# Kernel tuning notes

Measured on AMD Instinct MI355X. Metric: run time of the kernel, lower is better.

The kernel has to match this reference:

```python
import jax, jax.numpy as jnp
import numpy as np

DIM = 256
HEADS = 8
DIM_HEAD = 64
INNER = HEADS * DIM_HEAD  # 512
SCALE = DIM_HEAD ** -0.5


def setup_inputs() -> dict:
    key = jax.random.key(0)
    ks = jax.random.split(key, 6)
    b, n, m = 8, 2048, 16
    x = jax.random.normal(ks[0], (b, n, DIM), dtype=jnp.float32)
    y = jax.random.normal(ks[1], (b, n, m, DIM), dtype=jnp.float32)
    # nn.Linear weights stored as [out, in] in torch; we use [in, out] for x @ W
    W_q = jax.random.normal(ks[2], (DIM, INNER), dtype=jnp.float32) * (DIM ** -0.5)
    W_kv = jax.random.normal(ks[3], (DIM, 2 * INNER), dtype=jnp.float32) * (DIM ** -0.5)
    W_out = jax.random.normal(ks[4], (INNER, DIM), dtype=jnp.float32) * (INNER ** -0.5)
    b_out = jax.random.normal(ks[5], (DIM,), dtype=jnp.float32) * 0.01
    return {"x": x, "y": y, "W_q": W_q, "W_kv": W_kv, "W_out": W_out, "b_out": b_out}


def reference(x, y, W_q, W_kv, W_out, b_out):
    b, n, m, _ = y.shape
    h, d = HEADS, DIM_HEAD
    q = (x @ W_q).reshape(b, n, h, d)                      # [b,n,h,d] (single query per position)
    kv = y @ W_kv                                          # [b,n,m,2*inner]
    k, v = jnp.split(kv, 2, axis=-1)
    k = k.reshape(b, n, m, h, d)
    v = v.reshape(b, n, m, h, d)
    dots = jnp.einsum('bnhd,bnmhd->bnhm', q, k) * SCALE    # scores over m context tokens
    attn = jax.nn.softmax(dots, axis=-1)
    out = jnp.einsum('bnhm,bnmhd->bnhd', attn, v).reshape(b, n, h * d)
    return out @ W_out + b_out                             # [b,n,dim]
```

## Files before the change

kernel.cpp:

```cpp
#include <hip/hip_runtime.h>
#include <cmath>

#define NPOS 16384
#define ATT_SCALE 0.125f

typedef float f4 __attribute__((ext_vector_type(4)));
typedef short short8 __attribute__((ext_vector_type(8)));
typedef unsigned int uint;
typedef unsigned short ushort;

__device__ __forceinline__ ushort f2bf(float f) {
    union { float f; uint u; } v; v.f = f;
    uint r = v.u + 0x7fffu + ((v.u >> 16) & 1u);
    return (ushort)(r >> 16);
}
__device__ __forceinline__ float bfl(uint u) { union { uint u; float f; } v; v.u = u << 16; return v.f; }
__device__ __forceinline__ float bfh(uint u) { union { uint u; float f; } v; v.u = u & 0xffff0000u; return v.f; }

__device__ __forceinline__ void gl_lds16(const ushort* g, ushort* l) {
    __builtin_amdgcn_global_load_lds(
        (const __attribute__((address_space(1))) uint*)g,
        (__attribute__((address_space(3))) uint*)l, 16, 0, 0);
}

template<int BN, bool C_F32, bool BIAS>
__global__ __launch_bounds__(256) void gemm_bt(
    const ushort* __restrict__ A, int lda,
    const ushort* __restrict__ Bt, int ldb,
    void* __restrict__ Cg, int ldc,
    const float* __restrict__ bias, int K)
{
    constexpr int NI = BN / 32;
    __shared__ __align__(16) ushort A_lds[128 * 64];
    __shared__ __align__(16) ushort B_lds[BN * 64];
    const int mt = blockIdx.x, nt = blockIdx.y;
    const int row0 = mt * 128, col0 = nt * BN;
    const int tid = threadIdx.x;
    const int lane = tid & 63, w = tid >> 6;
    const int frow = lane & 15, quad = lane >> 4;
    const int wr = (w >> 1) * 64, wc = (w & 1) * (BN / 2);
    const int srow = lane >> 3;
    const int gch = ((lane & 7) ^ (lane >> 3)) * 8;

    f4 acc[4][NI];
    #pragma unroll
    for (int mi = 0; mi < 4; ++mi)
        #pragma unroll
        for (int ni = 0; ni < NI; ++ni)
            acc[mi][ni] = (f4){0.f, 0.f, 0.f, 0.f};

    for (int k0 = 0; k0 < K; k0 += 64) {
        #pragma unroll
        for (int it = 0; it < 4; ++it) {
            int sr = (it * 4 + w) * 8;
            gl_lds16(A + (size_t)(row0 + sr + srow) * lda + k0 + gch,
                     &A_lds[sr * 64]);
        }
        #pragma unroll
        for (int it = 0; it < BN / 32; ++it) {
            int sr = (it * 4 + w) * 8;
            gl_lds16(Bt + (size_t)(col0 + sr + srow) * ldb + k0 + gch,
                     &B_lds[sr * 64]);
        }
        __syncthreads();

        #pragma unroll
        for (int kk = 0; kk < 2; ++kk) {
            const int ko = (((kk * 4 + quad) ^ (frow & 7)) << 3);
            short8 av[4];
            #pragma unroll
            for (int mi = 0; mi < 4; ++mi)
                av[mi] = *(const short8*)&A_lds[(wr + mi * 16 + frow) * 64 + ko];
            #pragma unroll
            for (int ni = 0; ni < NI; ++ni) {
                short8 bv = *(const short8*)&B_lds[(wc + ni * 16 + frow) * 64 + ko];
                #pragma unroll
                for (int mi = 0; mi < 4; ++mi)
                    acc[mi][ni] = __builtin_amdgcn_mfma_f32_16x16x32_bf16(bv, av[mi], acc[mi][ni], 0, 0, 0);
            }
        }
        __syncthreads();
    }

    #pragma unroll
    for (int mi = 0; mi < 4; ++mi) {
        const int r = row0 + wr + mi * 16 + frow;
        #pragma unroll
        for (int ni = 0; ni < NI; ++ni) {
            const int c = col0 + wc + ni * 16 + quad * 4;
            f4 v = acc[mi][ni];
            if (C_F32) {
                float* C = (float*)Cg;
                if (BIAS) {
                    const float4 bv = *(const float4*)&bias[c];
                    v[0] += bv.x; v[1] += bv.y; v[2] += bv.z; v[3] += bv.w;
                }
                *(float4*)&C[(size_t)r * ldc + c] = make_float4(v[0], v[1], v[2], v[3]);
            } else {
                ushort* C = (ushort*)Cg;
                uint2 pv;
                pv.x = (uint)f2bf(v[0]) | ((uint)f2bf(v[1]) << 16);
                pv.y = (uint)f2bf(v[2]) | ((uint)f2bf(v[3]) << 16);
                *(uint2*)&C[(size_t)r * ldc + c] = pv;
            }
        }
    }
}

__global__ __launch_bounds__(256) void prep_all(
    const float* __restrict__ x, ushort* __restrict__ xb,
    const float* __restrict__ Wq, const float* __restrict__ Wkv,
    const float* __restrict__ Wout,
    ushort* __restrict__ Wf1n, ushort* __restrict__ Wf2t)
{
    __shared__ float As[64][65];
    __shared__ float Bs[64][65];

    if (blockIdx.x >= 256) {
        const int i = ((blockIdx.x - 256) * 256 + threadIdx.x) * 8;
        float4 v0 = *(const float4*)&x[i];
        float4 v1 = *(const float4*)&x[i + 4];
        uint4 p;
        p.x = (uint)f2bf(v0.x) | ((uint)f2bf(v0.y) << 16);
        p.y = (uint)f2bf(v0.z) | ((uint)f2bf(v0.w) << 16);
        p.z = (uint)f2bf(v1.x) | ((uint)f2bf(v1.y) << 16);
        p.w = (uint)f2bf(v1.z) | ((uint)f2bf(v1.w) << 16);
        *(uint4*)&xb[i] = p;
        return;
    }

    const int b = blockIdx.x;
    const bool second = (b >= 128);
    const int bb = second ? b - 128 : b;
    const int h = bb >> 4, ct = (bb >> 2) & 3, et = bb & 3;
    const int t = threadIdx.x;
    const int c0 = ct * 64, e0 = et * 64;
    const int tx = t & 15, ty = t >> 4;

    const float* Ab = Wkv + (second ? 512 : 0) + h * 64;
    #pragma unroll
    for (int it = 0; it < 4; ++it) {
        int idx = t + it * 256;
        int row = idx >> 4, col = (idx & 15) * 4;
        float4 v = *(const float4*)&Ab[(size_t)(c0 + row) * 1024 + col];
        As[row][col] = v.x; As[row][col + 1] = v.y;
        As[row][col + 2] = v.z; As[row][col + 3] = v.w;
    }
    #pragma unroll
    for (int it = 0; it < 4; ++it) {
        int idx = t + it * 256;
        int row = idx >> 4, col = (idx & 15) * 4;
        float4 v;
        if (second)
            v = *(const float4*)&Wout[(size_t)(h * 64 + row) * 256 + e0 + col];
        else
            v = *(const float4*)&Wq[(size_t)(e0 + row) * 512 + h * 64 + col];
        Bs[row][col] = v.x; Bs[row][col + 1] = v.y;
        Bs[row][col + 2] = v.z; Bs[row][col + 3] = v.w;
    }
    __syncthreads();

    float acc[4][4] = {};
    if (!second) {
        for (int k = 0; k < 64; ++k) {
            float a[4], bb2[4];
            #pragma unroll
            for (int i = 0; i < 4; ++i) a[i] = As[ty * 4 + i][k];
            #pragma unroll
            for (int j = 0; j < 4; ++j) bb2[j] = Bs[tx * 4 + j][k];
            #pragma unroll
            for (int i = 0; i < 4; ++i)
                #pragma unroll
                for (int j = 0; j < 4; ++j)
                    acc[i][j] = fmaf(a[i], bb2[j], acc[i][j]);
        }
        #pragma unroll
        for (int i = 0; i < 4; ++i) {
            int c = c0 + ty * 4 + i;
            uint2 pv;
            pv.x = (uint)f2bf(acc[i][0]) | ((uint)f2bf(acc[i][1]) << 16);
            pv.y = (uint)f2bf(acc[i][2]) | ((uint)f2bf(acc[i][3]) << 16);
            *(uint2*)&Wf1n[(size_t)(h * 256 + c) * 256 + e0 + tx * 4] = pv;
        }
    } else {
        for (int k = 0; k < 64; ++k) {
            float a[4], bb2[4];
            #pragma unroll
            for (int j = 0; j < 4; ++j) a[j] = As[tx * 4 + j][k];
            #pragma unroll
            for (int i = 0; i < 4; ++i) bb2[i] = Bs[k][ty * 4 + i];
            #pragma unroll
            for (int i = 0; i < 4; ++i)
                #pragma unroll
                for (int j = 0; j < 4; ++j)
                    acc[i][j] = fmaf(bb2[i], a[j], acc[i][j]);
        }
        #pragma unroll
        for (int i = 0; i < 4; ++i) {
            int e = e0 + ty * 4 + i;
            uint2 pv;
            pv.x = (uint)f2bf(acc[i][0]) | ((uint)f2bf(acc[i][1]) << 16);
            pv.y = (uint)f2bf(acc[i][2]) | ((uint)f2bf(acc[i][3]) << 16);
            *(uint2*)&Wf2t[(size_t)e * 2048 + h * 256 + c0 + tx * 4] = pv;
        }
    }
}

__global__ __launch_bounds__(256) void attn_k(
    const float* __restrict__ y, ushort* __restrict__ qk)
{
    __shared__ float ylds[16 * 260];
    __shared__ float qkf[8 * 260];
    __shared__ float part[4][8][16];
    __shared__ __align__(16) float attn_sT[16][8];
    const int p = blockIdx.x;
    const int t = threadIdx.x;
    const int w = t >> 6, lane = t & 63;
    const float* yp = y + (size_t)p * 4096;
    ushort* qkp = qk + (size_t)p * 2048;

    #pragma unroll
    for (int it = 0; it < 4; ++it) {
        int i = t + it * 256;
        float4 v = ((const float4*)yp)[i];
        int m = i >> 6, c4 = (i & 63) * 4;
        *(float4*)&ylds[m * 260 + c4] = v;
    }
    #pragma unroll
    for (int it = 0; it < 2; ++it) {
        int i = t + it * 256;
        uint2 v = ((const uint2*)qkp)[i];
        int h = i >> 6, c4 = (i & 63) * 4;
        float4 f = make_float4(bfl(v.x), bfh(v.x), bfl(v.y), bfh(v.y));
        *(float4*)&qkf[h * 260 + c4] = f;
    }
    __syncthreads();

    {
        const int m = t & 15, cs = t >> 4;
        float ps[8] = {0.f, 0.f, 0.f, 0.f, 0.f, 0.f, 0.f, 0.f};
        #pragma unroll
        for (int jj = 0; jj < 4; ++jj) {
            float4 yv = *(const float4*)&ylds[m * 260 + cs * 16 + jj * 4];
            #pragma unroll
            for (int h = 0; h < 8; ++h) {
                float4 qv = *(const float4*)&qkf[h * 260 + cs * 16 + jj * 4];
                ps[h] += yv.x * qv.x + yv.y * qv.y + yv.z * qv.z + yv.w * qv.w;
            }
        }
        #pragma unroll
        for (int h = 0; h < 8; ++h) {
            float s = ps[h];
            s += __shfl_xor(s, 16);
            s += __shfl_xor(s, 32);
            if (lane < 16) part[w][h][m] = s;
        }
    }
    __syncthreads();

    if (t < 128) {
        const int h = t >> 4, mm = t & 15;
        float d = (part[0][h][mm] + part[1][h][mm] + part[2][h][mm] + part[3][h][mm]) * ATT_SCALE;
        float mx = d;
        #pragma unroll
        for (int off = 8; off >= 1; off >>= 1) mx = fmaxf(mx, __shfl_xor(mx, off));
        float e = __expf(d - mx);
        float sm = e;
        #pragma unroll
        for (int off = 8; off >= 1; off >>= 1) sm += __shfl_xor(sm, off);
        attn_sT[mm][h] = e / sm;
    }
    __syncthreads();

    {
        float acc[8] = {0.f, 0.f, 0.f, 0.f, 0.f, 0.f, 0.f, 0.f};
        #pragma unroll
        for (int mm = 0; mm < 16; ++mm) {
            float yv = ylds[mm * 260 + t];
            float4 a0 = *(const float4*)&attn_sT[mm][0];
            float4 a1 = *(const float4*)&attn_sT[mm][4];
            acc[0] = fmaf(a0.x, yv, acc[0]);
            acc[1] = fmaf(a0.y, yv, acc[1]);
            acc[2] = fmaf(a0.z, yv, acc[2]);
            acc[3] = fmaf(a0.w, yv, acc[3]);
            acc[4] = fmaf(a1.x, yv, acc[4]);
            acc[5] = fmaf(a1.y, yv, acc[5]);
            acc[6] = fmaf(a1.z, yv, acc[6]);
            acc[7] = fmaf(a1.w, yv, acc[7]);
        }
        #pragma unroll
        for (int h = 0; h < 8; ++h) qkp[h * 256 + t] = f2bf(acc[h]);
    }
}

extern "C" void kernel_launch(void* const* d_in, const int* in_sizes, int n_in,
                              void* d_out, int out_size, void* d_ws, size_t ws_size,
                              hipStream_t stream)
{
    (void)in_sizes; (void)n_in; (void)out_size; (void)ws_size;
    const float* x     = (const float*)d_in[0];
    const float* y     = (const float*)d_in[1];
    const float* W_q   = (const float*)d_in[2];
    const float* W_kv  = (const float*)d_in[3];
    const float* W_out = (const float*)d_in[4];
    const float* b_out = (const float*)d_in[5];
    float* out = (float*)d_out;

    ushort* qk   = (ushort*)d_ws;
    ushort* xb   = qk + (size_t)NPOS * 2048;
    ushort* Wf1n = xb + (size_t)NPOS * 256;
    ushort* Wf2t = Wf1n + 2048 * 256;

    dim3 blk(256);

    prep_all<<<dim3(2304), blk, 0, stream>>>(x, xb, W_q, W_kv, W_out, Wf1n, Wf2t);

    gemm_bt<128, false, false><<<dim3(128, 16), blk, 0, stream>>>(
        xb, 256, Wf1n, 256, qk, 2048, nullptr, 256);

    attn_k<<<dim3(NPOS), blk, 0, stream>>>(y, qk);

    gemm_bt<64, true, true><<<dim3(128, 4), blk, 0, stream>>>(
        qk, 2048, Wf2t, 2048, out, 256, b_out, 2048);
}
```

Before: 466.6 us.

## Double-buffer LDS tiles in GEMM to overlap global loads with MFMA

Changes the bf16 GEMM main loop to use two LDS buffers for the A and B tiles. The next k-tile is prefetched via global_load_lds while the current one is computed, using explicit vmcnt waits and raw s_barrier. The wave priority is also raised during the MFMA section. This is meant to hide global memory latency, at the cost of twice the shared memory, which may lower occupancy. The hand-counted vmcnt values are fragile if the number of loads changes.

Measured after the change: 466.5 us. About the same (-0.0%).

```diff
diff --git a/kernel.cpp b/kernel.cpp
--- a/kernel.cpp
+++ b/kernel.cpp
@@ -31,10 +31,10 @@
     const float* __restrict__ bias, int K)
 {
     constexpr int NI = BN / 32;
-    __shared__ __align__(16) ushort A_lds[128 * 64];
-    __shared__ __align__(16) ushort B_lds[BN * 64];
-    const int mt = blockIdx.x, nt = blockIdx.y;
-    const int row0 = mt * 128, col0 = nt * BN;
+    __shared__ __align__(16) ushort A_lds[2][128 * 64];
+    __shared__ __align__(16) ushort B_lds[2][BN * 64];
+    const int mt = blockIdx.x, nt_b = blockIdx.y;
+    const int row0 = mt * 128, col0 = nt_b * BN;
     const int tid = threadIdx.x;
     const int lane = tid & 63, w = tid >> 6;
     const int frow = lane & 15, quad = lane >> 4;
@@ -49,37 +49,52 @@
         for (int ni = 0; ni < NI; ++ni)
             acc[mi][ni] = (f4){0.f, 0.f, 0.f, 0.f};
 
-    for (int k0 = 0; k0 < K; k0 += 64) {
+    auto stage = [&](int buf, int k0) {
         #pragma unroll
         for (int it = 0; it < 4; ++it) {
             int sr = (it * 4 + w) * 8;
             gl_lds16(A + (size_t)(row0 + sr + srow) * lda + k0 + gch,
-                     &A_lds[sr * 64]);
+                     &A_lds[buf][sr * 64]);
         }
         #pragma unroll
         for (int it = 0; it < BN / 32; ++it) {
             int sr = (it * 4 + w) * 8;
             gl_lds16(Bt + (size_t)(col0 + sr + srow) * ldb + k0 + gch,
-                     &B_lds[sr * 64]);
-        }
-        __syncthreads();
-
+                     &B_lds[buf][sr * 64]);
+        }
+    };
+
+    const int nsteps = K >> 6;
+    stage(0, 0);
+    for (int t = 0; t < nsteps; ++t) {
+        const int cbuf = t & 1;
+        if (t + 1 < nsteps) {
+            stage(cbuf ^ 1, (t + 1) << 6);
+            if constexpr (BN == 128) asm volatile("s_waitcnt vmcnt(8)" ::: "memory");
+            else                     asm volatile("s_waitcnt vmcnt(6)" ::: "memory");
+        } else {
+            asm volatile("s_waitcnt vmcnt(0)" ::: "memory");
+        }
+        __builtin_amdgcn_s_barrier();
+
+        __builtin_amdgcn_s_setprio(1);
         #pragma unroll
         for (int kk = 0; kk < 2; ++kk) {
             const int ko = (((kk * 4 + quad) ^ (frow & 7)) << 3);
             short8 av[4];
             #pragma unroll
             for (int mi = 0; mi < 4; ++mi)
-                av[mi] = *(const short8*)&A_lds[(wr + mi * 16 + frow) * 64 + ko];
+                av[mi] = *(const short8*)&A_lds[cbuf][(wr + mi * 16 + frow) * 64 + ko];
             #pragma unroll
             for (int ni = 0; ni < NI; ++ni) {
-                short8 bv = *(const short8*)&B_lds[(wc + ni * 16 + frow) * 64 + ko];
+                short8 bv = *(const short8*)&B_lds[cbuf][(wc + ni * 16 + frow) * 64 + ko];
                 #pragma unroll
                 for (int mi = 0; mi < 4; ++mi)
                     acc[mi][ni] = __builtin_amdgcn_mfma_f32_16x16x32_bf16(bv, av[mi], acc[mi][ni], 0, 0, 0);
             }
         }
-        __syncthreads();
+        __builtin_amdgcn_s_setprio(0);
+        __builtin_amdgcn_s_barrier();
     }
 
     #pragma unroll
```
